# Performance work log

Measured on AMD Instinct MI355X. Metric: run time of the kernel, lower is better.

Reference implementation:

```python
import jax, jax.numpy as jnp
import numpy as np

B, N, C_IN, C_OUT, HID = 2, 512, 16, 16, 64


def setup_inputs() -> dict:
    key = jax.random.key(0)
    ks = jax.random.split(key, 6)
    return {
        "features": jax.random.normal(ks[0], (B, N, C_IN), dtype=jnp.float32),
        "geometry": jax.random.normal(ks[1], (B, N, 3), dtype=jnp.float32),
        "W1": jax.random.normal(ks[2], (HID, 4), dtype=jnp.float32) * 0.5,
        "b1": jax.random.normal(ks[3], (HID,), dtype=jnp.float32) * 0.1,
        "W2": jax.random.normal(ks[4], (C_OUT * C_IN, HID), dtype=jnp.float32) * 0.1,
        "b2": jax.random.normal(ks[5], (C_OUT * C_IN,), dtype=jnp.float32) * 0.1,
    }


def reference(features, geometry, W1, b1, W2, b2):
    # rb = geometry.unsqueeze(1) -> [z,1,b,xyz]; ra = geometry.unsqueeze(2) -> [z,a,1,xyz]
    rel = geometry[:, None, :, :] - geometry[:, :, None, :]  # [z, a, b, 3] = rb - ra
    # kernel network: MLP on (rel, |rel|) -> [z, a, b, C_out, C_in]
    r2 = jnp.sum(rel * rel, axis=-1, keepdims=True)
    norm = jnp.sqrt(r2 + 1e-12)                              # differentiable at 0
    feat = jnp.concatenate([rel, norm], axis=-1)             # [z, a, b, 4]
    h = jax.nn.gelu(jnp.einsum('zabf,hf->zabh', feat, W1) + b1)
    k = (jnp.einsum('zabh,oh->zabo', h, W2) + b2)            # [z, a, b, C_out*C_in]
    z, a, b = k.shape[:3]
    k = k.reshape(z, a, b, C_OUT, C_IN)
    # contraction: torch.einsum('zabij,zbj->zabi')
    return jnp.einsum('zabij,zbj->zabi', k, features)
```

## Files before the change

### kernel.cpp

```cpp
#include <hip/hip_runtime.h>

#define NQ   512
#define CI   16
#define CO   16
#define HIDN 64

typedef __attribute__((ext_vector_type(8))) short bf16x8;
typedef __attribute__((ext_vector_type(4))) float f32x4;

__device__ __forceinline__ unsigned cvt_pk_bf16(float a, float b) {
    unsigned r;
    asm("v_cvt_pk_bf16_f32 %0, %1, %2" : "=v"(r) : "v"(a), "v"(b));
    return r;
}

__global__ __launch_bounds__(256, 4) void fused_mfma_kernel(
    const float* __restrict__ features,
    const float* __restrict__ geometry,
    const float* __restrict__ W1,
    const float* __restrict__ b1,
    const float* __restrict__ W2,
    const float* __restrict__ b2,
    float* __restrict__ out)
{
    __shared__ __attribute__((aligned(16))) float M_sm[CO][68];
    __shared__ float c_sm[CO];
    __shared__ float f_sm[CI];

    const int bid = blockIdx.x;
    const int zb  = bid >> 1;
    const int a0  = (bid & 1) << 8;
    const int z   = zb >> 9;
    const int b   = zb & 511;
    const int tid = threadIdx.x;

    if (tid < CI) f_sm[tid] = features[zb * CI + tid];
    __syncthreads();

    const int wv   = tid >> 6;
    const int lane = tid & 63;
    const int col  = lane & 15;
    const int g    = lane >> 4;
    const int abase = a0 + wv * 64;

    const float gbx = geometry[(z * NQ + b) * 3 + 0];
    const float gby = geometry[(z * NQ + b) * 3 + 1];
    const float gbz = geometry[(z * NQ + b) * 3 + 2];
    float rel[4][4];
    #pragma unroll
    for (int t = 0; t < 4; ++t) {
        const float* ga = geometry + (size_t)(z * NQ + abase + t * 16 + col) * 3;
        float rx = gbx - ga[0], ry = gby - ga[1], rz = gbz - ga[2];
        rel[t][0] = rx; rel[t][1] = ry; rel[t][2] = rz;
        rel[t][3] = sqrtf(fmaf(rx, rx, fmaf(ry, ry, rz * rz)) + 1e-12f);
    }

    {
        const int i  = tid >> 4;
        const int k4 = (tid & 15) * 4;
        float4 acc = {0.f, 0.f, 0.f, 0.f};
        #pragma unroll
        for (int j = 0; j < CI; ++j) {
            const float fj = f_sm[j];
            const float4 w2 = *reinterpret_cast<const float4*>(&W2[(i * CI + j) * HIDN + k4]);
            acc.x = fmaf(fj, w2.x, acc.x);
            acc.y = fmaf(fj, w2.y, acc.y);
            acc.z = fmaf(fj, w2.z, acc.z);
            acc.w = fmaf(fj, w2.w, acc.w);
        }
        *reinterpret_cast<float4*>(&M_sm[i][k4]) = acc;
    }
    if (tid < CO) {
        float acc = 0.f;
        #pragma unroll
        for (int j = 0; j < CI; ++j)
            acc = fmaf(f_sm[j], b2[tid * CI + j], acc);
        c_sm[tid] = acc;
    }
    __syncthreads();

    bf16x8 Af[2][2];
    #pragma unroll
    for (int kc = 0; kc < 2; ++kc) {
        const float* mp = &M_sm[col][kc * 32 + g * 8];
        unsigned hpk[4], lpk[4];
        #pragma unroll
        for (int p = 0; p < 4; ++p) {
            float m0 = mp[2 * p], m1 = mp[2 * p + 1];
            unsigned h = cvt_pk_bf16(m0, m1);
            float h0 = __builtin_bit_cast(float, h << 16);
            float h1 = __builtin_bit_cast(float, h & 0xffff0000u);
            hpk[p] = h;
            lpk[p] = cvt_pk_bf16(m0 - h0, m1 - h1);
        }
        union { unsigned u[4]; bf16x8 v; } uh, ul;
        #pragma unroll
        for (int p = 0; p < 4; ++p) { uh.u[p] = hpk[p]; ul.u[p] = lpk[p]; }
        Af[0][kc] = uh.v;
        Af[1][kc] = ul.v;
    }

    f32x4 cin;
    #pragma unroll
    for (int r = 0; r < 4; ++r) cin[r] = c_sm[g * 4 + r];
    f32x4 acc[4];
    #pragma unroll
    for (int t = 0; t < 4; ++t) acc[t] = cin;

    #pragma unroll
    for (int kc = 0; kc < 2; ++kc) {
        float4 w[8]; float bb[8];
        #pragma unroll
        for (int j = 0; j < 8; ++j) {
            int h = kc * 32 + g * 8 + j;
            w[j]  = *reinterpret_cast<const float4*>(W1 + h * 4);
            bb[j] = b1[h];
        }
        #pragma unroll
        for (int t = 0; t < 4; ++t) {
            float hv[8];
            #pragma unroll
            for (int j = 0; j < 8; ++j) {
                float x = bb[j];
                x = fmaf(rel[t][0], w[j].x, x);
                x = fmaf(rel[t][1], w[j].y, x);
                x = fmaf(rel[t][2], w[j].z, x);
                x = fmaf(rel[t][3], w[j].w, x);
                float q = fmaf(x * x, 0.044715f, 1.0f);
                float e = __builtin_amdgcn_exp2f((-2.3022082f * x) * q);
                hv[j]   = x * __builtin_amdgcn_rcpf(1.0f + e);
            }
            union { unsigned u[4]; bf16x8 v; } ua;
            #pragma unroll
            for (int p = 0; p < 4; ++p)
                ua.u[p] = cvt_pk_bf16(hv[2 * p], hv[2 * p + 1]);
            acc[t] = __builtin_amdgcn_mfma_f32_16x16x32_bf16(Af[0][kc], ua.v, acc[t], 0, 0, 0);
            acc[t] = __builtin_amdgcn_mfma_f32_16x16x32_bf16(Af[1][kc], ua.v, acc[t], 0, 0, 0);
        }
    }

    #pragma unroll
    for (int t = 0; t < 4; ++t) {
        float* op = out + (((size_t)(z * NQ + abase + t * 16 + col)) * NQ + b) * CO + g * 4;
        *reinterpret_cast<f32x4*>(op) = acc[t];
    }
}

extern "C" void kernel_launch(void* const* d_in, const int* in_sizes, int n_in,
                              void* d_out, int out_size, void* d_ws, size_t ws_size,
                              hipStream_t stream) {
    const float* features = (const float*)d_in[0];
    const float* geometry = (const float*)d_in[1];
    const float* W1       = (const float*)d_in[2];
    const float* b1       = (const float*)d_in[3];
    const float* W2       = (const float*)d_in[4];
    const float* b2       = (const float*)d_in[5];
    float* out = (float*)d_out;

    fused_mfma_kernel<<<2048, 256, 0, stream>>>(
        features, geometry, W1, b1, W2, b2, out);
}
```

Before: 26.74 us.

## Process two b columns per block with 128 a rows each

Measured after the change: 28.43 us. +6.3%, slower.

```diff
diff --git a/kernel.cpp b/kernel.cpp
--- a/kernel.cpp
+++ b/kernel.cpp
@@ -14,7 +14,7 @@
     return r;
 }
 
-__global__ __launch_bounds__(256, 4) void fused_mfma_kernel(
+__global__ __launch_bounds__(256, 3) void fused_mfma_kernel(
     const float* __restrict__ features,
     const float* __restrict__ geometry,
     const float* __restrict__ W1,
@@ -23,126 +23,154 @@
     const float* __restrict__ b2,
     float* __restrict__ out)
 {
-    __shared__ __attribute__((aligned(16))) float M_sm[CO][68];
-    __shared__ float c_sm[CO];
-    __shared__ float f_sm[CI];
+    __shared__ __attribute__((aligned(16))) float M_sm[2][CO][68];
+    __shared__ float c_sm[2][CO];
+    __shared__ float f_sm[2][CI];
 
     const int bid = blockIdx.x;
-    const int zb  = bid >> 1;
-    const int a0  = (bid & 1) << 8;
-    const int z   = zb >> 9;
-    const int b   = zb & 511;
+    const int bp  = bid >> 2;
+    const int aq  = bid & 3;
+    const int z   = bp >> 8;
+    const int b0  = (bp & 255) << 1;
     const int tid = threadIdx.x;
 
-    if (tid < CI) f_sm[tid] = features[zb * CI + tid];
+    if (tid < 32) {
+        const int bb = tid >> 4, j = tid & 15;
+        f_sm[bb][j] = features[(z * NQ + b0 + bb) * CI + j];
+    }
     __syncthreads();
 
-    const int wv   = tid >> 6;
-    const int lane = tid & 63;
-    const int col  = lane & 15;
-    const int g    = lane >> 4;
-    const int abase = a0 + wv * 64;
+    const int wv    = tid >> 6;
+    const int lane  = tid & 63;
+    const int col   = lane & 15;
+    const int g     = lane >> 4;
+    const int abase = aq * 128 + wv * 32;
 
-    const float gbx = geometry[(z * NQ + b) * 3 + 0];
-    const float gby = geometry[(z * NQ + b) * 3 + 1];
-    const float gbz = geometry[(z * NQ + b) * 3 + 2];
-    float rel[4][4];
+    float gax[2], gay[2], gaz[2];
     #pragma unroll
-    for (int t = 0; t < 4; ++t) {
+    for (int t = 0; t < 2; ++t) {
         const float* ga = geometry + (size_t)(z * NQ + abase + t * 16 + col) * 3;
-        float rx = gbx - ga[0], ry = gby - ga[1], rz = gbz - ga[2];
-        rel[t][0] = rx; rel[t][1] = ry; rel[t][2] = rz;
-        rel[t][3] = sqrtf(fmaf(rx, rx, fmaf(ry, ry, rz * rz)) + 1e-12f);
+        gax[t] = ga[0]; gay[t] = ga[1]; gaz[t] = ga[2];
+    }
+    float rel[2][2][4];
+    #pragma unroll
+    for (int bb = 0; bb < 2; ++bb) {
+        const float gbx = geometry[(z * NQ + b0 + bb) * 3 + 0];
+        const float gby = geometry[(z * NQ + b0 + bb) * 3 + 1];
+        const float gbz = geometry[(z * NQ + b0 + bb) * 3 + 2];
+        #pragma unroll
+        for (int t = 0; t < 2; ++t) {
+            float rx = gbx - gax[t], ry = gby - gay[t], rz = gbz - gaz[t];
+            rel[t][bb][0] = rx; rel[t][bb][1] = ry; rel[t][bb][2] = rz;
+            rel[t][bb][3] = sqrtf(fmaf(rx, rx, fmaf(ry, ry, rz * rz)) + 1e-12f);
+        }
     }
 
     {
         const int i  = tid >> 4;
         const int k4 = (tid & 15) * 4;
-        float4 acc = {0.f, 0.f, 0.f, 0.f};
+        f32x4 a0v = {0.f, 0.f, 0.f, 0.f};
+        f32x4 a1v = {0.f, 0.f, 0.f, 0.f};
         #pragma unroll
         for (int j = 0; j < CI; ++j) {
-            const float fj = f_sm[j];
-            const float4 w2 = *reinterpret_cast<const float4*>(&W2[(i * CI + j) * HIDN + k4]);
-            acc.x = fmaf(fj, w2.x, acc.x);
-            acc.y = fmaf(fj, w2.y, acc.y);
-            acc.z = fmaf(fj, w2.z, acc.z);
-            acc.w = fmaf(fj, w2.w, acc.w);
+            const f32x4 w2 = *reinterpret_cast<const f32x4*>(&W2[(i * CI + j) * HIDN + k4]);
+            const float f0 = f_sm[0][j], f1 = f_sm[1][j];
+            #pragma unroll
+            for (int p = 0; p < 4; ++p) {
+                a0v[p] = fmaf(f0, w2[p], a0v[p]);
+                a1v[p] = fmaf(f1, w2[p], a1v[p]);
+            }
         }
-        *reinterpret_cast<float4*>(&M_sm[i][k4]) = acc;
+        *reinterpret_cast<f32x4*>(&M_sm[0][i][k4]) = a0v;
+        *reinterpret_cast<f32x4*>(&M_sm[1][i][k4]) = a1v;
     }
-    if (tid < CO) {
+    if (tid < 32) {
+        const int bb = tid >> 4, i = tid & 15;
         float acc = 0.f;
         #pragma unroll
         for (int j = 0; j < CI; ++j)
-            acc = fmaf(f_sm[j], b2[tid * CI + j], acc);
-        c_sm[tid] = acc;
+            acc = fmaf(f_sm[bb][j], b2[i * CI + j], acc);
+        c_sm[bb][i] = acc;
     }
     __syncthreads();
 
-    bf16x8 Af[2][2];
+    bf16x8 Af[2][2][2];
     #pragma unroll
-    for (int kc = 0; kc < 2; ++kc) {
-        const float* mp = &M_sm[col][kc * 32 + g * 8];
-        unsigned hpk[4], lpk[4];
+    for (int bb = 0; bb < 2; ++bb) {
         #pragma unroll
-        for (int p = 0; p < 4; ++p) {
-            float m0 = mp[2 * p], m1 = mp[2 * p + 1];
-            unsigned h = cvt_pk_bf16(m0, m1);
-            float h0 = __builtin_bit_cast(float, h << 16);
-            float h1 = __builtin_bit_cast(float, h & 0xffff0000u);
-            hpk[p] = h;
-            lpk[p] = cvt_pk_bf16(m0 - h0, m1 - h1);
+        for (int kc = 0; kc < 2; ++kc) {
+            const float* mp = &M_sm[bb][col][kc * 32 + g * 8];
+            unsigned hpk[4], lpk[4];
+            #pragma unroll
+            for (int p = 0; p < 4; ++p) {
+                float m0 = mp[2 * p], m1 = mp[2 * p + 1];
+                unsigned h = cvt_pk_bf16(m0, m1);
+                float h0 = __builtin_bit_cast(float, h << 16);
+                float h1 = __builtin_bit_cast(float, h & 0xffff0000u);
+                hpk[p] = h;
+                lpk[p] = cvt_pk_bf16(m0 - h0, m1 - h1);
+            }
+            union { unsigned u[4]; bf16x8 v; } uh, ul;
+            #pragma unroll
+            for (int p = 0; p < 4; ++p) { uh.u[p] = hpk[p]; ul.u[p] = lpk[p]; }
+            Af[bb][0][kc] = uh.v;
+            Af[bb][1][kc] = ul.v;
         }
-        union { unsigned u[4]; bf16x8 v; } uh, ul;
-        #pragma unroll
-        for (int p = 0; p < 4; ++p) { uh.u[p] = hpk[p]; ul.u[p] = lpk[p]; }
-        Af[0][kc] = uh.v;
-        Af[1][kc] = ul.v;
     }
 
-    f32x4 cin;
+    f32x4 cin[2];
     #pragma unroll
-    for (int r = 0; r < 4; ++r) cin[r] = c_sm[g * 4 + r];
-    f32x4 acc[4];
+    for (int bb = 0; bb < 2; ++bb)
+        #pragma unroll
+        for (int r = 0; r < 4; ++r) cin[bb][r] = c_sm[bb][g * 4 + r];
+    f32x4 acc[2][2];
     #pragma unroll
-    for (int t = 0; t < 4; ++t) acc[t] = cin;
+    for (int t = 0; t < 2; ++t)
+        #pragma unroll
+        for (int bb = 0; bb < 2; ++bb) acc[t][bb] = cin[bb];
 
     #pragma unroll
     for (int kc = 0; kc < 2; ++kc) {
-        float4 w[8]; float bb[8];
+        float4 w[8]; float bbias[8];
         #pragma unroll
         for (int j = 0; j < 8; ++j) {
-            int h = kc * 32 + g * 8 + j;
-            w[j]  = *reinterpret_cast<const float4*>(W1 + h * 4);
-            bb[j] = b1[h];
+            const int h = kc * 32 + g * 8 + j;
+            w[j]     = *reinterpret_cast<const float4*>(W1 + h * 4);
+            bbias[j] = b1[h];
         }
         #pragma unroll
-        for (int t = 0; t < 4; ++t) {
-            float hv[8];
+        for (int t = 0; t < 2; ++t) {
             #pragma unroll
-            for (int j = 0; j < 8; ++j) {
-                float x = bb[j];
-                x = fmaf(rel[t][0], w[j].x, x);
-                x = fmaf(rel[t][1], w[j].y, x);
-                x = fmaf(rel[t][2], w[j].z, x);
-                x = fmaf(rel[t][3], w[j].w, x);
-                float q = fmaf(x * x, 0.044715f, 1.0f);
-                float e = __builtin_amdgcn_exp2f((-2.3022082f * x) * q);
-                hv[j]   = x * __builtin_amdgcn_rcpf(1.0f + e);
+            for (int bb = 0; bb < 2; ++bb) {
+                float hv[8];
+                #pragma unroll
+                for (int j = 0; j < 8; ++j) {
+                    float x = bbias[j];
+                    x = fmaf(rel[t][bb][0], w[j].x, x);
+                    x = fmaf(rel[t][bb][1], w[j].y, x);
+                    x = fmaf(rel[t][bb][2], w[j].z, x);
+                    x = fmaf(rel[t][bb][3], w[j].w, x);
+                    float q = fmaf(x * x, 0.044715f, 1.0f);
+                    float e = __builtin_amdgcn_exp2f((-2.3022082f * x) * q);
+                    hv[j]   = x * __builtin_amdgcn_rcpf(1.0f + e);
+                }
+                union { unsigned u[4]; bf16x8 v; } ua;
+                #pragma unroll
+                for (int p = 0; p < 4; ++p)
+                    ua.u[p] = cvt_pk_bf16(hv[2 * p], hv[2 * p + 1]);
+                acc[t][bb] = __builtin_amdgcn_mfma_f32_16x16x32_bf16(Af[bb][0][kc], ua.v, acc[t][bb], 0, 0, 0);
+                acc[t][bb] = __builtin_amdgcn_mfma_f32_16x16x32_bf16(Af[bb][1][kc], ua.v, acc[t][bb], 0, 0, 0);
             }
-            union { unsigned u[4]; bf16x8 v; } ua;
-            #pragma unroll
-            for (int p = 0; p < 4; ++p)
-                ua.u[p] = cvt_pk_bf16(hv[2 * p], hv[2 * p + 1]);
-            acc[t] = __builtin_amdgcn_mfma_f32_16x16x32_bf16(Af[0][kc], ua.v, acc[t], 0, 0, 0);
-            acc[t] = __builtin_amdgcn_mfma_f32_16x16x32_bf16(Af[1][kc], ua.v, acc[t], 0, 0, 0);
         }
     }
 
     #pragma unroll
-    for (int t = 0; t < 4; ++t) {
-        float* op = out + (((size_t)(z * NQ + abase + t * 16 + col)) * NQ + b) * CO + g * 4;
-        *reinterpret_cast<f32x4*>(op) = acc[t];
+    for (int t = 0; t < 2; ++t) {
+        #pragma unroll
+        for (int bb = 0; bb < 2; ++bb) {
+            float* op = out + (((size_t)(z * NQ + abase + t * 16 + col)) * NQ + (b0 + bb)) * CO + g * 4;
+            *reinterpret_cast<f32x4*>(op) = acc[t][bb];
+        }
     }
 }
 
```
